# Kernel optimization log

Measured on AMD Instinct MI355X. Metric: run time of the kernel, lower is better.

Reference implementation:

```python
import jax, jax.numpy as jnp
import numpy as np

N_NODES = 100000
N_EDGES = 1600000
IN_CH = 128
HEADS = 4
OUT_CH = 32
EPS_BN = 1e-5


def setup_inputs() -> dict:
    key = jax.random.key(0)
    ks = jax.random.split(key, 8)
    s = 1.0 / np.sqrt(IN_CH)
    return {
        "x": jax.random.normal(ks[0], (N_NODES, IN_CH), jnp.float32),
        "edge_index": jax.random.randint(ks[1], (2, N_EDGES), 0, N_NODES, jnp.int32),
        "W_src": jax.random.normal(ks[2], (IN_CH, HEADS * OUT_CH), jnp.float32) * s,
        "W_dst": jax.random.normal(ks[3], (IN_CH, HEADS * OUT_CH), jnp.float32) * s,
        "att": jax.random.normal(ks[4], (HEADS, OUT_CH), jnp.float32) * s,
        "bias": jnp.zeros((HEADS * OUT_CH,), jnp.float32),
        "bn_gamma": jnp.ones((HEADS * OUT_CH,), jnp.float32),
        "bn_beta": jnp.zeros((HEADS * OUT_CH,), jnp.float32),
    }


def reference(x, edge_index, W_src, W_dst, att, bias, bn_gamma, bn_beta):
    N = x.shape[0]
    H, C = att.shape
    # add self-loops (PyG default add_self_loops=True)
    loop = jnp.arange(N, dtype=edge_index.dtype)
    src = jnp.concatenate([edge_index[0], loop])  # source j
    dst = jnp.concatenate([edge_index[1], loop])  # destination i

    h_src = (x @ W_src).reshape(N, H, C)
    h_dst = (x @ W_dst).reshape(N, H, C)

    # GATv2 edge scores: a^T LeakyReLU(h_src[j] + h_dst[i]), slope 0.2
    e = jax.nn.leaky_relu(h_src[src] + h_dst[dst], 0.2)  # [E+N, H, C]
    logits = jnp.einsum('ehc,hc->eh', e, att)            # [E+N, H]

    # segment softmax over incoming edges of each destination node
    m = jax.ops.segment_max(logits, dst, num_segments=N)  # [N, H]
    ex = jnp.exp(logits - m[dst])
    denom = jax.ops.segment_sum(ex, dst, num_segments=N)  # [N, H] (>0 via self-loops)
    alpha = ex / denom[dst]                                # [E+N, H]

    # weighted scatter-sum aggregation of source features
    out = jax.ops.segment_sum(alpha[:, :, None] * h_src[src], dst, num_segments=N)
    out = out.reshape(N, H * C) + bias

    # BatchNorm1d (training-mode batch statistics) + LeakyReLU(0.02)
    mean = out.mean(axis=0)
    var = out.var(axis=0)
    y = bn_gamma * (out - mean) * jax.lax.rsqrt(var + EPS_BN) + bn_beta
    return jax.nn.leaky_relu(y, 0.02)
```

## Files before the change

kernel.cpp:

```cpp
#include <hip/hip_runtime.h>
#include <math.h>

#define N_IN   128
#define HC     128
#define HEADS  4
#define PB_T   4096
#define PB_THR 512
#define CAP    8192
#define STB    1024

typedef __attribute__((ext_vector_type(2))) __fp16 f16x2;
typedef __attribute__((ext_vector_type(8))) __fp16 f16x8;
typedef __attribute__((ext_vector_type(4))) float f32x4;

__device__ __forceinline__ unsigned f16pk(float a, float b) {
    f16x2 r = __builtin_amdgcn_cvt_pkrtz(a, b);
    return __builtin_bit_cast(unsigned, r);
}

__global__ __launch_bounds__(256) void k_prep(const float* __restrict__ Ws,
        const float* __restrict__ Wd, unsigned short* __restrict__ Wt) {
    int i = blockIdx.x * 256 + threadIdx.x;
    if (i >= 256 * 128) return;
    int n = i >> 7, k = i & 127;
    float v = (n < 128) ? Ws[k * HC + n] : Wd[k * HC + (n - 128)];
    __fp16 h = (__fp16)v;
    Wt[i] = __builtin_bit_cast(unsigned short, h);
}

__global__ __launch_bounds__(256) void k_gemm(const float* __restrict__ x,
        const __fp16* __restrict__ Wt,
        unsigned short* __restrict__ hs, unsigned short* __restrict__ hd, int N) {
    int wave = threadIdx.x >> 6, lane = threadIdx.x & 63;
    int chbase = wave * 64;
    int nbase = blockIdx.x * 32;
    int lr = lane & 15;
    int lg = lane >> 4;

    f16x8 a[4][4];
#pragma unroll
    for (int ct = 0; ct < 4; ct++)
#pragma unroll
        for (int kk = 0; kk < 4; kk++)
            a[ct][kk] = *reinterpret_cast<const f16x8*>(
                &Wt[(size_t)(chbase + ct * 16 + lr) * 128 + kk * 32 + lg * 8]);

    f32x4 acc[2][4];
#pragma unroll
    for (int rt = 0; rt < 2; rt++)
#pragma unroll
        for (int ct = 0; ct < 4; ct++)
            acc[rt][ct] = (f32x4){0.f, 0.f, 0.f, 0.f};

#pragma unroll
    for (int rt = 0; rt < 2; rt++) {
        int node = nbase + rt * 16 + lr;
        const float* xr = x + (size_t)node * N_IN;
        bool ok = (node < N);
        f16x8 bfr[4];
#pragma unroll
        for (int kk = 0; kk < 4; kk++) {
            f32x4 xa = (f32x4){0.f, 0.f, 0.f, 0.f}, xb = xa;
            if (ok) {
                xa = *reinterpret_cast<const f32x4*>(xr + kk * 32 + lg * 8);
                xb = *reinterpret_cast<const f32x4*>(xr + kk * 32 + lg * 8 + 4);
            }
            uint4 u;
            u.x = f16pk(xa[0], xa[1]); u.y = f16pk(xa[2], xa[3]);
            u.z = f16pk(xb[0], xb[1]); u.w = f16pk(xb[2], xb[3]);
            bfr[kk] = __builtin_bit_cast(f16x8, u);
        }
#pragma unroll
        for (int kk = 0; kk < 4; kk++)
#pragma unroll
            for (int ct = 0; ct < 4; ct++)
                acc[rt][ct] = __builtin_amdgcn_mfma_f32_16x16x32_f16(
                    a[ct][kk], bfr[kk], acc[rt][ct], 0, 0, 0);
    }

#pragma unroll
    for (int rt = 0; rt < 2; rt++) {
        int node = nbase + rt * 16 + lr;
        if (node >= N) continue;
#pragma unroll
        for (int ct = 0; ct < 4; ct++) {
            int ch = chbase + ct * 16 + lg * 4;
            unsigned short* outp = (ch < HC) ? hs : hd;
            int cc = ch & (HC - 1);
            uint2 r;
            r.x = f16pk(acc[rt][ct][0], acc[rt][ct][1]);
            r.y = f16pk(acc[rt][ct][2], acc[rt][ct][3]);
            *reinterpret_cast<uint2*>(outp + (size_t)node * HC + cc) = r;
        }
    }
}

__global__ __launch_bounds__(PB_THR) void k_part(const int* __restrict__ ei,
        int* __restrict__ bcur, unsigned* __restrict__ ebuf, int E, int NB) {
    __shared__ int cnt[512], lscan[512], gbase[512], lcnt[512];
    __shared__ unsigned pr[PB_T];
    __shared__ unsigned short pb[PB_T];
    int t = threadIdx.x;
    int tb = blockIdx.x * PB_T;
    int tc = min(PB_T, E - tb);
    cnt[t] = 0; lcnt[t] = 0;
    __syncthreads();
    int dd[8], ss[8];
#pragma unroll
    for (int i = 0; i < 8; i++) {
        int e = tb + t + i * PB_THR;
        if (e < E) {
            ss[i] = ei[e];
            dd[i] = ei[E + e];
            atomicAdd(&cnt[dd[i] >> 8], 1);
        } else dd[i] = -1;
    }
    __syncthreads();
    lscan[t] = cnt[t];
    __syncthreads();
    for (int ofs = 1; ofs < 512; ofs <<= 1) {
        int add = (t >= ofs) ? lscan[t - ofs] : 0;
        __syncthreads();
        lscan[t] += add;
        __syncthreads();
    }
    if (t < NB && cnt[t] > 0) gbase[t] = atomicAdd(&bcur[t], cnt[t]);
    __syncthreads();
#pragma unroll
    for (int i = 0; i < 8; i++) {
        if (dd[i] >= 0) {
            int b = dd[i] >> 8;
            int lpos = atomicAdd(&lcnt[b], 1);
            int j = lscan[b] - cnt[b] + lpos;
            pr[j] = ((unsigned)ss[i] << 8) | (unsigned)(dd[i] & 255);
            pb[j] = (unsigned short)b;
        }
    }
    __syncthreads();
    for (int k = t; k < tc; k += PB_THR) {
        int b = pb[k];
        ebuf[(size_t)b * CAP + gbase[b] + k - (lscan[b] - cnt[b])] = pr[k];
    }
}

__global__ __launch_bounds__(256) void k_place(const unsigned* __restrict__ ebuf,
        const int* __restrict__ bcur, int* __restrict__ deg, int* __restrict__ off,
        int* __restrict__ ssrc, int N) {
    __shared__ int hist[256], loff[256];
    int b = blockIdx.x;
    int t = threadIdx.x;
    int base = b * CAP;
    int cntb = bcur[b];
    hist[t] = 0;
    __syncthreads();
    for (int k = t; k < cntb; k += 256)
        atomicAdd(&hist[ebuf[base + k] & 255u], 1);
    __syncthreads();
    int v = hist[t];
    loff[t] = v;
    __syncthreads();
    for (int ofs = 1; ofs < 256; ofs <<= 1) {
        int add = (t >= ofs) ? loff[t - ofs] : 0;
        __syncthreads();
        loff[t] += add;
        __syncthreads();
    }
    int excl = loff[t] - v;
    int node = (b << 8) + t;
    if (node < N) { deg[node] = v; off[node] = base + excl; }
    hist[t] = base + excl;
    __syncthreads();
    for (int k = t; k < cntb; k += 256) {
        unsigned u = ebuf[base + k];
        int pos = atomicAdd(&hist[u & 255u], 1);
        ssrc[pos] = (int)(u & 0xFFFFFF00u);
    }
}

__global__ __launch_bounds__(256) void k_agg2(const unsigned short* __restrict__ hs,
        const unsigned short* __restrict__ hd, const int* __restrict__ off,
        const int* __restrict__ deg, const int* __restrict__ ssrc,
        const float* __restrict__ att, unsigned* __restrict__ outh,
        int N, int NP) {
    int b = blockIdx.x;
    int H = (b >> 2) & 1;
    int j = (b >> 3) * 4 + (b & 3);
    int pair = j * 4 + (threadIdx.x >> 6);
    if (pair >= NP) return;
    int lane = threadIdx.x & 63;
    int g  = lane >> 5;
    int e  = (lane >> 3) & 3;
    int cb = lane & 7;
    int node = pair * 2 + g;
    if (node >= N) return;

    unsigned rowoff = (unsigned)(H * 128 + cb * 16);
    const unsigned char* hsb = (const unsigned char*)hs;
    const unsigned char* hdb = (const unsigned char*)hd;

    int chbase = H * 64 + cb * 8;
    f32x4 a0 = *reinterpret_cast<const f32x4*>(att + chbase);
    f32x4 a1 = *reinterpret_cast<const f32x4*>(att + chbase + 4);
    f16x2 at2[4];
    at2[0] = __builtin_bit_cast(f16x2, f16pk(a0[0], a0[1]));
    at2[1] = __builtin_bit_cast(f16x2, f16pk(a0[2], a0[3]));
    at2[2] = __builtin_bit_cast(f16x2, f16pk(a1[0], a1[1]));
    at2[3] = __builtin_bit_cast(f16x2, f16pk(a1[2], a1[3]));

    uint4 hu = *reinterpret_cast<const uint4*>(hdb + (size_t)node * 256u + rowoff);
    f16x2 hdv[4];
    hdv[0] = __builtin_bit_cast(f16x2, hu.x);
    hdv[1] = __builtin_bit_cast(f16x2, hu.y);
    hdv[2] = __builtin_bit_cast(f16x2, hu.z);
    hdv[3] = __builtin_bit_cast(f16x2, hu.w);

    float acc[8];
#pragma unroll
    for (int k = 0; k < 8; k++) acc[k] = 0.f;
    float ssum = 0.f;
    const f16x2 c02 = {(__fp16)0.2f, (__fp16)0.2f};

    auto process = [&](unsigned byteoff) {
        uint4 u = *reinterpret_cast<const uint4*>(hsb + byteoff);
        f16x2 v[4];
        v[0] = __builtin_bit_cast(f16x2, u.x);
        v[1] = __builtin_bit_cast(f16x2, u.y);
        v[2] = __builtin_bit_cast(f16x2, u.z);
        v[3] = __builtin_bit_cast(f16x2, u.w);
        float p = 0.f;
#pragma unroll
        for (int k = 0; k < 4; k++) {
            f16x2 s = v[k] + hdv[k];
            f16x2 t = __builtin_elementwise_max(s, s * c02);
            p = __builtin_amdgcn_fdot2(t, at2[k], p, false);
        }
        p += __shfl_xor(p, 1);
        p += __shfl_xor(p, 2);
        float ee = __expf(p);
        ssum += ee;
#pragma unroll
        for (int k = 0; k < 4; k++) {
            acc[2 * k]     += ee * (float)v[k][0];
            acc[2 * k + 1] += ee * (float)v[k][1];
        }
    };

    if (e == 0) process((unsigned)node * 256u + rowoff);
    int beg = off[node], end = beg + deg[node];
    for (int i = beg + e; i < end; i += 4)
        process((unsigned)ssrc[i] + rowoff);

    ssum += __shfl_xor(ssum, 8);
    ssum += __shfl_xor(ssum, 16);
#pragma unroll
    for (int k = 0; k < 8; k++) {
        acc[k] += __shfl_xor(acc[k], 8);
        acc[k] += __shfl_xor(acc[k], 16);
    }
    if (e == 0) {
        float inv = 1.f / ssum;
        uint4 r;
        r.x = f16pk(acc[0] * inv, acc[1] * inv);
        r.y = f16pk(acc[2] * inv, acc[3] * inv);
        r.z = f16pk(acc[4] * inv, acc[5] * inv);
        r.w = f16pk(acc[6] * inv, acc[7] * inv);
        *reinterpret_cast<uint4*>(outh + (size_t)node * 64 + H * 32 + cb * 4) = r;
    }
}

__global__ __launch_bounds__(256) void k_stats(const unsigned short* __restrict__ outh16,
        float* __restrict__ statp, int N) {
    int ch = threadIdx.x & 127;
    int half = threadIdx.x >> 7;
    float s = 0.f, s2 = 0.f;
    for (int n = blockIdx.x * 2 + half; n < N; n += gridDim.x * 2) {
        __fp16 h = __builtin_bit_cast(__fp16, outh16[(size_t)n * HC + ch]);
        float v = (float)h;
        s += v; s2 += v * v;
    }
    __shared__ float sh[2][256];
    sh[0][threadIdx.x] = s; sh[1][threadIdx.x] = s2;
    __syncthreads();
    if (threadIdx.x < 128) {
        size_t base = (size_t)blockIdx.x * 256;
        statp[base + threadIdx.x]       = sh[0][threadIdx.x] + sh[0][threadIdx.x + 128];
        statp[base + 128 + threadIdx.x] = sh[1][threadIdx.x] + sh[1][threadIdx.x + 128];
    }
}

__global__ __launch_bounds__(256) void k_redstats(const float* __restrict__ statp,
        float* __restrict__ stats, int NBLK) {
    int t = threadIdx.x;
    float acc = 0.f;
    for (int r = blockIdx.x; r < NBLK; r += gridDim.x)
        acc += statp[(size_t)r * 256 + t];
    atomicAdd(&stats[t], acc);
}

__global__ void k_bnparams(const float* __restrict__ stats,
        const float* __restrict__ gamma, const float* __restrict__ beta,
        float* __restrict__ ss, int N) {
    int c = threadIdx.x;
    if (c >= HC) return;
    float mean = stats[c] / (float)N;
    float var  = stats[HC + c] / (float)N - mean * mean;
    float sc = gamma[c] * rsqrtf(var + 1e-5f);
    ss[c]      = sc;
    ss[HC + c] = beta[c] - mean * sc;
}

__global__ __launch_bounds__(256) void k_final(const unsigned short* __restrict__ outh16,
        const float* __restrict__ ss, float* __restrict__ out, int total) {
    int i = blockIdx.x * 256 + threadIdx.x;
    if (i >= total) return;
    int c = i & 127;
    __fp16 h = __builtin_bit_cast(__fp16, outh16[i]);
    float y = (float)h * ss[c] + ss[HC + c];
    out[i] = (y > 0.f) ? y : 0.02f * y;
}

extern "C" void kernel_launch(void* const* d_in, const int* in_sizes, int n_in,
                              void* d_out, int out_size, void* d_ws, size_t ws_size,
                              hipStream_t stream) {
    const float* x     = (const float*)d_in[0];
    const int*   ei    = (const int*)d_in[1];
    const float* Ws    = (const float*)d_in[2];
    const float* Wd    = (const float*)d_in[3];
    const float* att   = (const float*)d_in[4];
    const float* gamma = (const float*)d_in[6];
    const float* beta  = (const float*)d_in[7];
    float* out = (float*)d_out;

    int N  = in_sizes[0] / N_IN;
    int E  = in_sizes[1] / 2;
    int NB = (N + 255) >> 8;
    int NP = (N + 1) / 2;
    int G4 = (NP + 3) / 4;
    int AGRID = 8 * ((G4 + 3) / 4);

    char* ws = (char*)d_ws;
    unsigned short* hs = (unsigned short*)ws; ws += (size_t)N * HC * 2;
    unsigned short* hd = (unsigned short*)ws; ws += (size_t)N * HC * 2;
    unsigned* outh = (unsigned*)ws; ws += (size_t)N * HC * 2;
    int* deg    = (int*)ws;      ws += (size_t)N * 4;
    int* off    = (int*)ws;      ws += (size_t)N * 4;
    unsigned* ebuf = (unsigned*)ws; ws += (size_t)NB * CAP * 4;
    int* ssrc   = (int*)ws;      ws += (size_t)NB * CAP * 4;
    int* bcur   = (int*)ws;      ws += (size_t)NB * 4;
    unsigned short* Wt = (unsigned short*)ws; ws += 256 * 128 * 2;
    float* statp= (float*)ws;    ws += (size_t)STB * 256 * 4;
    float* stats= (float*)ws;    ws += 2 * HC * 4;
    float* ss   = (float*)ws;    ws += 2 * HC * 4;

    hipMemsetAsync(bcur, 0, (size_t)NB * 4, stream);
    hipMemsetAsync(stats, 0, 2 * HC * 4, stream);

    k_prep<<<128, 256, 0, stream>>>(Ws, Wd, Wt);
    k_gemm<<<(N + 31) / 32, 256, 0, stream>>>(x, (const __fp16*)Wt, hs, hd, N);
    k_part<<<(E + PB_T - 1) / PB_T, PB_THR, 0, stream>>>(ei, bcur, ebuf, E, NB);
    k_place<<<NB, 256, 0, stream>>>(ebuf, bcur, deg, off, ssrc, N);
    k_agg2<<<AGRID, 256, 0, stream>>>(hs, hd, off, deg, ssrc, att, outh, N, NP);
    k_stats<<<STB, 256, 0, stream>>>((const unsigned short*)outh, statp, N);
    k_redstats<<<64, 256, 0, stream>>>(statp, stats, STB);
    k_bnparams<<<1, 128, 0, stream>>>(stats, gamma, beta, ss, N);
    k_final<<<(N * HC + 255) / 256, 256, 0, stream>>>((const unsigned short*)outh, ss, out, N * HC);
}
```

Measured before the change: 239.6 us.

## Fold memsets into prep, widen place block, vectorize stats and final

Zeroing of the bucket counters and the stats accumulator moves into the k_prep kernel, which removes two memset launches. k_place now runs 512 threads per block so each bucket is histogrammed and scattered by twice as many threads. k_stats reads packed half2 words, and k_final reads four halves and writes a float4 per thread, which widens memory accesses and cuts the thread count in the bandwidth-bound tail kernels. Together these are meant to trim launch overhead and per-element memory traffic cost.

```diff
diff --git a/kernel.cpp b/kernel.cpp
--- a/kernel.cpp
+++ b/kernel.cpp
@@ -17,10 +17,18 @@
     f16x2 r = __builtin_amdgcn_cvt_pkrtz(a, b);
     return __builtin_bit_cast(unsigned, r);
 }
+__device__ __forceinline__ float2 h2f(unsigned u) {
+    f16x2 h = __builtin_bit_cast(f16x2, u);
+    return make_float2((float)h[0], (float)h[1]);
+}
 
 __global__ __launch_bounds__(256) void k_prep(const float* __restrict__ Ws,
-        const float* __restrict__ Wd, unsigned short* __restrict__ Wt) {
-    int i = blockIdx.x * 256 + threadIdx.x;
+        const float* __restrict__ Wd, unsigned short* __restrict__ Wt,
+        float* __restrict__ stats, int* __restrict__ bcur, int NB) {
+    int t = threadIdx.x;
+    if (blockIdx.x == 0) stats[t] = 0.f;
+    if (blockIdx.x == 1) for (int i = t; i < NB; i += 256) bcur[i] = 0;
+    int i = blockIdx.x * 256 + t;
     if (i >= 256 * 128) return;
     int n = i >> 7, k = i & 127;
     float v = (n < 128) ? Ws[k * HC + n] : Wd[k * HC + (n - 128)];
@@ -143,7 +151,7 @@
     }
 }
 
-__global__ __launch_bounds__(256) void k_place(const unsigned* __restrict__ ebuf,
+__global__ __launch_bounds__(512) void k_place(const unsigned* __restrict__ ebuf,
         const int* __restrict__ bcur, int* __restrict__ deg, int* __restrict__ off,
         int* __restrict__ ssrc, int N) {
     __shared__ int hist[256], loff[256];
@@ -151,26 +159,28 @@
     int t = threadIdx.x;
     int base = b * CAP;
     int cntb = bcur[b];
-    hist[t] = 0;
-    __syncthreads();
-    for (int k = t; k < cntb; k += 256)
+    if (t < 256) hist[t] = 0;
+    __syncthreads();
+    for (int k = t; k < cntb; k += 512)
         atomicAdd(&hist[ebuf[base + k] & 255u], 1);
     __syncthreads();
-    int v = hist[t];
-    loff[t] = v;
+    int v = (t < 256) ? hist[t] : 0;
+    if (t < 256) loff[t] = v;
     __syncthreads();
     for (int ofs = 1; ofs < 256; ofs <<= 1) {
-        int add = (t >= ofs) ? loff[t - ofs] : 0;
+        int add = (t < 256 && t >= ofs) ? loff[t - ofs] : 0;
         __syncthreads();
-        loff[t] += add;
+        if (t < 256) loff[t] += add;
         __syncthreads();
     }
-    int excl = loff[t] - v;
-    int node = (b << 8) + t;
-    if (node < N) { deg[node] = v; off[node] = base + excl; }
-    hist[t] = base + excl;
-    __syncthreads();
-    for (int k = t; k < cntb; k += 256) {
+    if (t < 256) {
+        int excl = loff[t] - v;
+        int node = (b << 8) + t;
+        if (node < N) { deg[node] = v; off[node] = base + excl; }
+        hist[t] = base + excl;
+    }
+    __syncthreads();
+    for (int k = t; k < cntb; k += 512) {
         unsigned u = ebuf[base + k];
         int pos = atomicAdd(&hist[u & 255u], 1);
         ssrc[pos] = (int)(u & 0xFFFFFF00u);
@@ -268,23 +278,31 @@
     }
 }
 
-__global__ __launch_bounds__(256) void k_stats(const unsigned short* __restrict__ outh16,
+__global__ __launch_bounds__(256) void k_stats(const unsigned* __restrict__ outh32,
         float* __restrict__ statp, int N) {
-    int ch = threadIdx.x & 127;
-    int half = threadIdx.x >> 7;
-    float s = 0.f, s2 = 0.f;
-    for (int n = blockIdx.x * 2 + half; n < N; n += gridDim.x * 2) {
-        __fp16 h = __builtin_bit_cast(__fp16, outh16[(size_t)n * HC + ch]);
-        float v = (float)h;
-        s += v; s2 += v * v;
-    }
-    __shared__ float sh[2][256];
-    sh[0][threadIdx.x] = s; sh[1][threadIdx.x] = s2;
-    __syncthreads();
-    if (threadIdx.x < 128) {
+    int q = threadIdx.x >> 6;
+    int u = threadIdx.x & 63;
+    float s0 = 0.f, s1 = 0.f, q0 = 0.f, q1 = 0.f;
+    for (int n = blockIdx.x * 4 + q; n < N; n += gridDim.x * 4) {
+        float2 v = h2f(outh32[(size_t)n * 64 + u]);
+        s0 += v.x; s1 += v.y;
+        q0 += v.x * v.x; q1 += v.y * v.y;
+    }
+    __shared__ float sh[4][256];
+    sh[0][threadIdx.x] = s0; sh[1][threadIdx.x] = s1;
+    sh[2][threadIdx.x] = q0; sh[3][threadIdx.x] = q1;
+    __syncthreads();
+    if (threadIdx.x < 64) {
         size_t base = (size_t)blockIdx.x * 256;
-        statp[base + threadIdx.x]       = sh[0][threadIdx.x] + sh[0][threadIdx.x + 128];
-        statp[base + 128 + threadIdx.x] = sh[1][threadIdx.x] + sh[1][threadIdx.x + 128];
+        int t = threadIdx.x;
+        float a0 = sh[0][t] + sh[0][t + 64] + sh[0][t + 128] + sh[0][t + 192];
+        float a1 = sh[1][t] + sh[1][t + 64] + sh[1][t + 128] + sh[1][t + 192];
+        float b0 = sh[2][t] + sh[2][t + 64] + sh[2][t + 128] + sh[2][t + 192];
+        float b1 = sh[3][t] + sh[3][t + 64] + sh[3][t + 128] + sh[3][t + 192];
+        statp[base + 2 * t]       = a0;
+        statp[base + 2 * t + 1]   = a1;
+        statp[base + 128 + 2 * t]     = b0;
+        statp[base + 128 + 2 * t + 1] = b1;
     }
 }
 
@@ -309,14 +327,23 @@
     ss[HC + c] = beta[c] - mean * sc;
 }
 
-__global__ __launch_bounds__(256) void k_final(const unsigned short* __restrict__ outh16,
-        const float* __restrict__ ss, float* __restrict__ out, int total) {
+__global__ __launch_bounds__(256) void k_final(const uint2* __restrict__ outh64,
+        const float* __restrict__ ss, float* __restrict__ out, int nquad) {
     int i = blockIdx.x * 256 + threadIdx.x;
-    if (i >= total) return;
-    int c = i & 127;
-    __fp16 h = __builtin_bit_cast(__fp16, outh16[i]);
-    float y = (float)h * ss[c] + ss[HC + c];
-    out[i] = (y > 0.f) ? y : 0.02f * y;
+    if (i >= nquad) return;
+    int c = (i & 31) * 4;
+    uint2 v = outh64[i];
+    float2 v0 = h2f(v.x), v1 = h2f(v.y);
+    float y0 = v0.x * ss[c]     + ss[HC + c];
+    float y1 = v0.y * ss[c + 1] + ss[HC + c + 1];
+    float y2 = v1.x * ss[c + 2] + ss[HC + c + 2];
+    float y3 = v1.y * ss[c + 3] + ss[HC + c + 3];
+    f32x4 r;
+    r[0] = (y0 > 0.f) ? y0 : 0.02f * y0;
+    r[1] = (y1 > 0.f) ? y1 : 0.02f * y1;
+    r[2] = (y2 > 0.f) ? y2 : 0.02f * y2;
+    r[3] = (y3 > 0.f) ? y3 : 0.02f * y3;
+    *reinterpret_cast<f32x4*>(out + (size_t)i * 4) = r;
 }
 
 extern "C" void kernel_launch(void* const* d_in, const int* in_sizes, int n_in,
@@ -352,16 +379,13 @@
     float* stats= (float*)ws;    ws += 2 * HC * 4;
     float* ss   = (float*)ws;    ws += 2 * HC * 4;
 
-    hipMemsetAsync(bcur, 0, (size_t)NB * 4, stream);
-    hipMemsetAsync(stats, 0, 2 * HC * 4, stream);
-
-    k_prep<<<128, 256, 0, stream>>>(Ws, Wd, Wt);
+    k_prep<<<128, 256, 0, stream>>>(Ws, Wd, Wt, stats, bcur, NB);
     k_gemm<<<(N + 31) / 32, 256, 0, stream>>>(x, (const __fp16*)Wt, hs, hd, N);
     k_part<<<(E + PB_T - 1) / PB_T, PB_THR, 0, stream>>>(ei, bcur, ebuf, E, NB);
-    k_place<<<NB, 256, 0, stream>>>(ebuf, bcur, deg, off, ssrc, N);
+    k_place<<<NB, 512, 0, stream>>>(ebuf, bcur, deg, off, ssrc, N);
     k_agg2<<<AGRID, 256, 0, stream>>>(hs, hd, off, deg, ssrc, att, outh, N, NP);
-    k_stats<<<STB, 256, 0, stream>>>((const unsigned short*)outh, statp, N);
+    k_stats<<<STB, 256, 0, stream>>>(outh, statp, N);
     k_redstats<<<64, 256, 0, stream>>>(statp, stats, STB);
     k_bnparams<<<1, 128, 0, stream>>>(stats, gamma, beta, ss, N);
-    k_final<<<(N * HC + 255) / 256, 256, 0, stream>>>((const unsigned short*)outh, ss, out, N * HC);
-}
+    k_final<<<(N * HC / 4 + 255) / 256, 256, 0, stream>>>((const uint2*)outh, ss, out, N * HC / 4);
+}
```

Measured after the change: 213.7 us. -10.8%, faster.
